# Kernel optimization log

Hardware: AMD Instinct MI355X
Metric: run time of the kernel (lower is better)

## Reference

```python
import jax, jax.numpy as jnp
import numpy as np
from jax import lax

B, T, D, N = 64, 4096, 256, 64


def setup_inputs() -> dict:
    key = jax.random.key(0)
    ks = jax.random.split(key, 3)
    return {
        "x": jax.random.normal(ks[0], (B, T, D), dtype=jnp.float32),
        "mask": jnp.ones((B, T), dtype=bool),
        "W": jax.random.normal(ks[1], (D, N), dtype=jnp.float32) * (1.0 / np.sqrt(D)),
        "b": jnp.zeros((N,), dtype=jnp.float32),
        "trans": jax.random.normal(ks[2], (N, N), dtype=jnp.float32) * 0.1,
        "left_boundary": jnp.zeros((N,), dtype=jnp.float32),
        "right_boundary": jnp.zeros((N,), dtype=jnp.float32),
    }


def _viterbi_decode(potentials, lens, trans):
    # potentials: [B, T, N]; lens: [B] int32; trans: [N, N]
    Tt = potentials.shape[1]

    def fwd_step(state, inp):
        pot_t, t = inp  # pot_t: [B, N], t scalar time index (1..T-1)
        scores = state[:, :, None] + trans[None, :, :]        # [B, N_prev, N_cur]
        bp = jnp.argmax(scores, axis=1).astype(jnp.int32)      # [B, N]
        new_state = pot_t + jnp.max(scores, axis=1)            # [B, N]
        valid = (t < lens)[:, None]                            # carry state past length
        return jnp.where(valid, new_state, state), bp

    pots_t = jnp.swapaxes(potentials, 0, 1)  # [T, B, N]
    final_state, bps = lax.scan(fwd_step, pots_t[0], (pots_t[1:], jnp.arange(1, Tt)))
    last_tag = jnp.argmax(final_state, axis=1).astype(jnp.int32)  # [B]

    def bwd_step(tag, inp):
        bp, t = inp  # bp: [B, N] backpointers for time t+1; t in 0..T-2
        prev = jnp.take_along_axis(bp, tag[:, None], axis=1)[:, 0]
        new_tag = jnp.where(t < lens - 1, prev, last_tag)
        return new_tag, new_tag

    _, tags = lax.scan(bwd_step, last_tag, (bps, jnp.arange(Tt - 1)), reverse=True)
    # tags: [T-1, B], position t holds decoded tag at time t
    decoded = jnp.concatenate([tags.T, last_tag[:, None]], axis=1)  # [B, T]
    return decoded


def reference(x, mask, W, b, trans, left_boundary, right_boundary):
    # projection (use_kernel=True)
    pot = jnp.einsum("btd,dn->btn", x, W) + b  # [B, T, N]
    # boundary potentials (use_boundary=True): added at fixed first/last timestep
    pot = pot.at[:, 0, :].add(left_boundary)
    pot = pot.at[:, -1, :].add(right_boundary)
    lens = jnp.sum(mask.astype(jnp.int32), axis=1)  # [B]
    decoded = _viterbi_decode(pot, lens, trans)
    return decoded, pot, lens, trans
```

## Files before the change

kernel.cpp:

```cpp
#include <hip/hip_runtime.h>

#define B_ 64
#define T_ 4096
#define D_ 256
#define N_ 64

typedef float f32x16 __attribute__((ext_vector_type(16)));

__global__ __launch_bounds__(64) void k_misc(const unsigned char* __restrict__ mask,
                                             const float* __restrict__ trans,
                                             float* __restrict__ out_lens,
                                             float* __restrict__ out_trans,
                                             int* __restrict__ lens_i) {
  int blk = blockIdx.x, lane = threadIdx.x;
  if (blk < B_) {
    int probe = (int)mask[0] + (int)mask[1] + (int)mask[2] + (int)mask[3];
    int cnt = 0;
    if (probe >= 2) {
      const unsigned char* row = mask + (size_t)blk * T_;
      for (int i = lane; i < T_; i += 64) cnt += row[i] ? 1 : 0;
    } else {
      const int* rowi = (const int*)mask + (size_t)blk * T_;
      for (int i = lane; i < T_; i += 64) cnt += rowi[i] ? 1 : 0;
    }
    #pragma unroll
    for (int off = 32; off > 0; off >>= 1) cnt += __shfl_down(cnt, off, 64);
    if (lane == 0) { out_lens[blk] = (float)cnt; lens_i[blk] = cnt; }
  } else {
    int base = (blk - B_) * 1024;
    for (int i = lane; i < 1024; i += 64) out_trans[base + i] = trans[base + i];
  }
}

__global__ __launch_bounds__(256, 2) void k_gemm(const float* __restrict__ x,
                                                 const float* __restrict__ W,
                                                 const float* __restrict__ bias,
                                                 const float* __restrict__ lb,
                                                 const float* __restrict__ rb,
                                                 float* __restrict__ pot) {
  __shared__ float xs[64 * D_];
  int tid = threadIdx.x;
  int wid = tid >> 6, lane = tid & 63;
  size_t row0 = (size_t)blockIdx.x * 64;

  const float* xb = x + row0 * D_;
  #pragma unroll
  for (int i = 0; i < 16; ++i) {
    int r = wid * 16 + i;
    float4 v = *reinterpret_cast<const float4*>(xb + (size_t)r * D_ + lane * 4);
    *reinterpret_cast<float4*>(&xs[r * D_ + lane * 4]) = v;
  }
  __syncthreads();

  float bv = bias[lane];
  float lbv = lb[lane];
  float rbv = rb[lane];

  float acc[16];
  #pragma unroll
  for (int r = 0; r < 16; ++r) {
    int t = (int)((row0 + wid * 16 + r) & (T_ - 1));
    float a = bv;
    if (t == 0)      a += lbv;
    if (t == T_ - 1) a += rbv;
    acc[r] = a;
  }

  #pragma unroll
  for (int c = 0; c < 4; ++c) {
    float w[64];
    #pragma unroll
    for (int k = 0; k < 64; ++k) w[k] = W[(size_t)(c * 64 + k) * N_ + lane];
    #pragma unroll
    for (int r = 0; r < 16; ++r) {
      const float4* xr = reinterpret_cast<const float4*>(&xs[(wid * 16 + r) * D_ + c * 64]);
      #pragma unroll
      for (int q = 0; q < 16; ++q) {
        float4 xv = xr[q];
        acc[r] += xv.x * w[q * 4 + 0];
        acc[r] += xv.y * w[q * 4 + 1];
        acc[r] += xv.z * w[q * 4 + 2];
        acc[r] += xv.w * w[q * 4 + 3];
      }
    }
  }

  #pragma unroll
  for (int r = 0; r < 16; ++r)
    pot[(row0 + wid * 16 + r) * N_ + lane] = acc[r];
}

#define FWD_STEP(TIDX, PREG)                                                      \
  {                                                                               \
    float pot_t = PREG;                                                           \
    int tp = (TIDX) + 4; if (tp > T_ - 1) tp = T_ - 1;                            \
    PREG = pb[(size_t)tp * N_ + lane];                                            \
    float m[64];                                                                  \
    _Pragma("unroll")                                                             \
    for (int g = 0; g < 16; ++g) {                                                \
      float4 s4 = st4v[g];                                                        \
      float2 ca = make_float2(s4.x, s4.y) + t2[2 * g];                            \
      float2 cb = make_float2(s4.z, s4.w) + t2[2 * g + 1];                        \
      m[4 * g + 0] = ca.x; m[4 * g + 1] = ca.y;                                   \
      m[4 * g + 2] = cb.x; m[4 * g + 3] = cb.y;                                   \
    }                                                                             \
    float r1[22];                                                                 \
    _Pragma("unroll")                                                             \
    for (int i = 0; i < 21; ++i)                                                  \
      r1[i] = fmaxf(fmaxf(m[3 * i], m[3 * i + 1]), m[3 * i + 2]);                 \
    r1[21] = m[63];                                                               \
    float r2[8];                                                                  \
    _Pragma("unroll")                                                             \
    for (int i = 0; i < 7; ++i)                                                   \
      r2[i] = fmaxf(fmaxf(r1[3 * i], r1[3 * i + 1]), r1[3 * i + 2]);              \
    r2[7] = r1[21];                                                               \
    float r3a = fmaxf(fmaxf(r2[0], r2[1]), r2[2]);                                \
    float r3b = fmaxf(fmaxf(r2[3], r2[4]), r2[5]);                                \
    float r3c = fmaxf(r2[6], r2[7]);                                              \
    float best = fmaxf(fmaxf(r3a, r3b), r3c);                                     \
    float ns = pot_t + best;                                                      \
    state = ((TIDX) < len_b) ? ns : state;                                        \
    sb[(size_t)(TIDX) * N_ + lane] = state;                                       \
    __builtin_amdgcn_wave_barrier();                                              \
    st[lane] = state;                                                             \
    __builtin_amdgcn_wave_barrier();                                              \
  }

__global__ __launch_bounds__(64, 1) void k_fwd_states(const float* __restrict__ pot,
                                                      const float* __restrict__ trans,
                                                      const int* __restrict__ lens_i,
                                                      float* __restrict__ states,
                                                      float* __restrict__ fstate) {
  int b = blockIdx.x, lane = threadIdx.x;
  __shared__ float4 st4v[16];
  float* st = (float*)st4v;

  float2 t2[32];
  #pragma unroll
  for (int p = 0; p < 32; ++p)
    t2[p] = make_float2(trans[(2 * p) * N_ + lane], trans[(2 * p + 1) * N_ + lane]);

  const float* pb = pot + (size_t)b * T_ * N_;
  float* sb = states + (size_t)b * T_ * N_;
  int len_b = lens_i[b];

  float state = pb[lane];
  st[lane] = state;
  sb[lane] = state;
  __builtin_amdgcn_wave_barrier();

  float p0 = pb[1 * N_ + lane];
  float p1 = pb[2 * N_ + lane];
  float p2 = pb[3 * N_ + lane];
  float p3 = pb[4 * N_ + lane];

  int t = 1;
  for (; t + 3 <= T_ - 1; t += 4) {
    FWD_STEP(t + 0, p0);
    FWD_STEP(t + 1, p1);
    FWD_STEP(t + 2, p2);
    FWD_STEP(t + 3, p3);
  }
  FWD_STEP(t + 0, p0);
  FWD_STEP(t + 1, p1);
  FWD_STEP(t + 2, p2);

  fstate[b * N_ + lane] = state;
}

__global__ __launch_bounds__(64, 2) void k_bp(const float* __restrict__ states,
                                              const float* __restrict__ trans,
                                              unsigned char* __restrict__ bp) {
  unsigned idx = blockIdx.x;
  unsigned b = idx / (unsigned)(T_ - 1);
  unsigned t = 1u + idx - b * (unsigned)(T_ - 1);
  int lane = threadIdx.x;

  float tcol[64];
  #pragma unroll
  for (int p = 0; p < 64; ++p) tcol[p] = trans[p * N_ + lane];

  const float* srow = states + ((size_t)b * T_ + (t - 1)) * N_;

  float c[64];
  #pragma unroll
  for (int p = 0; p < 64; ++p) c[p] = srow[p] + tcol[p];

  float v1[32]; int i1[32];
  #pragma unroll
  for (int i = 0; i < 32; ++i) {
    bool g = c[2 * i + 1] > c[2 * i];
    v1[i] = g ? c[2 * i + 1] : c[2 * i];
    i1[i] = g ? 2 * i + 1 : 2 * i;
  }
  float v2[16]; int i2[16];
  #pragma unroll
  for (int i = 0; i < 16; ++i) {
    bool g = v1[2 * i + 1] > v1[2 * i];
    v2[i] = g ? v1[2 * i + 1] : v1[2 * i];
    i2[i] = g ? i1[2 * i + 1] : i1[2 * i];
  }
  float v3[8]; int i3[8];
  #pragma unroll
  for (int i = 0; i < 8; ++i) {
    bool g = v2[2 * i + 1] > v2[2 * i];
    v3[i] = g ? v2[2 * i + 1] : v2[2 * i];
    i3[i] = g ? i2[2 * i + 1] : i2[2 * i];
  }
  float v4[4]; int i4[4];
  #pragma unroll
  for (int i = 0; i < 4; ++i) {
    bool g = v3[2 * i + 1] > v3[2 * i];
    v4[i] = g ? v3[2 * i + 1] : v3[2 * i];
    i4[i] = g ? i3[2 * i + 1] : i3[2 * i];
  }
  bool ga = v4[1] > v4[0];
  float va = ga ? v4[1] : v4[0]; int ia = ga ? i4[1] : i4[0];
  bool gb = v4[3] > v4[2];
  float vb = gb ? v4[3] : v4[2]; int ib = gb ? i4[3] : i4[2];
  int bpi = (vb > va) ? ib : ia;

  bp[((size_t)b * T_ + t) * N_ + lane] = (unsigned char)bpi;
}

__global__ __launch_bounds__(64, 1) void k_bwd(const unsigned char* __restrict__ bp,
                                               const float* __restrict__ fstate,
                                               const int* __restrict__ lens_i,
                                               float* __restrict__ decoded) {
  int b = blockIdx.x, lane = threadIdx.x;

  __shared__ float fv[64];
  __shared__ int sh_tag;
  fv[lane] = fstate[b * N_ + lane];
  __syncthreads();
  if (lane == 0) {
    float best = fv[0]; int tg = 0;
    for (int i = 1; i < 64; ++i) if (fv[i] > best) { best = fv[i]; tg = i; }
    sh_tag = tg;
  }
  __syncthreads();
  int s_last = __builtin_amdgcn_readfirstlane(sh_tag);
  int len_b = lens_i[b];

  const unsigned char* bpb = bp + (size_t)b * T_ * N_;
  float* dec = decoded + (size_t)b * T_;

  int s_tag = s_last;
  if (lane == 0) dec[T_ - 1] = (float)s_last;

  const int G = 32;
  int bufA[G], bufB[G];
  const int k0 = T_ - 1;
  #pragma unroll
  for (int i = 0; i < G; ++i) bufA[i] = (int)bpb[(size_t)(k0 - i) * N_ + lane];

  const int nrows = T_ - 1;
  const int groups = nrows / G;

  for (int g = 0; g < groups; ++g) {
    int kn = k0 - G * (g + 1);
    #pragma unroll
    for (int i = 0; i < G; ++i)
      bufB[i] = (kn - i >= 1) ? (int)bpb[(size_t)(kn - i) * N_ + lane] : 0;

    int kbase = k0 - G * g;
    #pragma unroll
    for (int i = 0; i < G; ++i) {
      int k = kbase - i;
      int prev = __builtin_amdgcn_readlane(bufA[i], s_tag);
      int t = k - 1;
      s_tag = (t < len_b - 1) ? prev : s_last;
      if (lane == 0) dec[t] = (float)s_tag;
    }
    #pragma unroll
    for (int i = 0; i < G; ++i) bufA[i] = bufB[i];
  }

  int kbase = k0 - G * groups;
  #pragma unroll
  for (int i = 0; i < G; ++i) {
    int k = kbase - i;
    if (k >= 1) {
      int prev = __builtin_amdgcn_readlane(bufA[i], s_tag);
      int t = k - 1;
      s_tag = (t < len_b - 1) ? prev : s_last;
      if (lane == 0) dec[t] = (float)s_tag;
    }
  }
}

extern "C" void kernel_launch(void* const* d_in, const int* in_sizes, int n_in,
                              void* d_out, int out_size, void* d_ws, size_t ws_size,
                              hipStream_t stream) {
  const float* x            = (const float*)d_in[0];
  const unsigned char* mask = (const unsigned char*)d_in[1];
  const float* W            = (const float*)d_in[2];
  const float* bias         = (const float*)d_in[3];
  const float* trans        = (const float*)d_in[4];
  const float* lb           = (const float*)d_in[5];
  const float* rb           = (const float*)d_in[6];

  float* out         = (float*)d_out;
  float* out_decoded = out;
  float* out_pot     = out + (size_t)B_ * T_;
  float* out_lens    = out_pot + (size_t)B_ * T_ * N_;
  float* out_trans   = out_lens + B_;

  const size_t bp_bytes   = (size_t)B_ * T_ * N_;
  const size_t fstate_off = bp_bytes;
  const size_t lens_off   = fstate_off + (size_t)B_ * N_ * 4;
  const size_t states_off = lens_off + 256;

  unsigned char* bp = (unsigned char*)d_ws;
  float* fstate     = (float*)((char*)d_ws + fstate_off);
  int*   lens_i     = (int*)((char*)d_ws + lens_off);
  float* states     = (float*)((char*)d_ws + states_off);

  k_misc<<<68, 64, 0, stream>>>(mask, trans, out_lens, out_trans, lens_i);
  k_gemm<<<(B_ * T_) / 64, 256, 0, stream>>>(x, W, bias, lb, rb, out_pot);
  k_fwd_states<<<B_, 64, 0, stream>>>(out_pot, trans, lens_i, states, fstate);
  k_bp<<<B_ * (T_ - 1), 64, 0, stream>>>(states, trans, bp);
  k_bwd<<<B_, 64, 0, stream>>>(bp, fstate, lens_i, out_decoded);
}
```

Baseline: 1.492 ms.

## Interleave two batch rows per forward wave and batch four timesteps per bp block

The forward max-plus recurrence kernel now runs one wave per pair of batch rows, interleaving two independent dependency chains so their LDS reads and max reductions can overlap. The goal is to hide per-step latency in the serial scan. The cost is half as many active waves (32 instead of 64), which leaves much of the GPU idle, and higher register pressure. The backpointer kernel now handles four timesteps per block, reusing the trans column it loads and cutting the block count by four, though this lowers parallelism in that kernel.

```diff
diff --git a/kernel.cpp b/kernel.cpp
--- a/kernel.cpp
+++ b/kernel.cpp
@@ -90,39 +90,59 @@
     pot[(row0 + wid * 16 + r) * N_ + lane] = acc[r];
 }
 
-#define FWD_STEP(TIDX, PREG)                                                      \
+#define FWD_STEP2(TIDX, PRA, PRB)                                                 \
   {                                                                               \
-    float pot_t = PREG;                                                           \
+    float potA = PRA;                                                             \
+    float potB = PRB;                                                             \
     int tp = (TIDX) + 4; if (tp > T_ - 1) tp = T_ - 1;                            \
-    PREG = pb[(size_t)tp * N_ + lane];                                            \
-    float m[64];                                                                  \
+    PRA = pbA[(size_t)tp * N_ + lane];                                            \
+    PRB = pbB[(size_t)tp * N_ + lane];                                            \
+    float mA[64], mB[64];                                                         \
     _Pragma("unroll")                                                             \
     for (int g = 0; g < 16; ++g) {                                                \
-      float4 s4 = st4v[g];                                                        \
+      float4 s4 = stA4[g];                                                        \
       float2 ca = make_float2(s4.x, s4.y) + t2[2 * g];                            \
       float2 cb = make_float2(s4.z, s4.w) + t2[2 * g + 1];                        \
-      m[4 * g + 0] = ca.x; m[4 * g + 1] = ca.y;                                   \
-      m[4 * g + 2] = cb.x; m[4 * g + 3] = cb.y;                                   \
+      mA[4 * g + 0] = ca.x; mA[4 * g + 1] = ca.y;                                 \
+      mA[4 * g + 2] = cb.x; mA[4 * g + 3] = cb.y;                                 \
     }                                                                             \
-    float r1[22];                                                                 \
     _Pragma("unroll")                                                             \
-    for (int i = 0; i < 21; ++i)                                                  \
-      r1[i] = fmaxf(fmaxf(m[3 * i], m[3 * i + 1]), m[3 * i + 2]);                 \
-    r1[21] = m[63];                                                               \
-    float r2[8];                                                                  \
+    for (int g = 0; g < 16; ++g) {                                                \
+      float4 s4 = stB4[g];                                                        \
+      float2 ca = make_float2(s4.x, s4.y) + t2[2 * g];                            \
+      float2 cb = make_float2(s4.z, s4.w) + t2[2 * g + 1];                        \
+      mB[4 * g + 0] = ca.x; mB[4 * g + 1] = ca.y;                                 \
+      mB[4 * g + 2] = cb.x; mB[4 * g + 3] = cb.y;                                 \
+    }                                                                             \
+    float r1A[22], r1B[22];                                                       \
     _Pragma("unroll")                                                             \
-    for (int i = 0; i < 7; ++i)                                                   \
-      r2[i] = fmaxf(fmaxf(r1[3 * i], r1[3 * i + 1]), r1[3 * i + 2]);              \
-    r2[7] = r1[21];                                                               \
-    float r3a = fmaxf(fmaxf(r2[0], r2[1]), r2[2]);                                \
-    float r3b = fmaxf(fmaxf(r2[3], r2[4]), r2[5]);                                \
-    float r3c = fmaxf(r2[6], r2[7]);                                              \
-    float best = fmaxf(fmaxf(r3a, r3b), r3c);                                     \
-    float ns = pot_t + best;                                                      \
-    state = ((TIDX) < len_b) ? ns : state;                                        \
-    sb[(size_t)(TIDX) * N_ + lane] = state;                                       \
+    for (int i = 0; i < 21; ++i) {                                                \
+      r1A[i] = fmaxf(fmaxf(mA[3 * i], mA[3 * i + 1]), mA[3 * i + 2]);             \
+      r1B[i] = fmaxf(fmaxf(mB[3 * i], mB[3 * i + 1]), mB[3 * i + 2]);             \
+    }                                                                             \
+    r1A[21] = mA[63]; r1B[21] = mB[63];                                           \
+    float r2A[8], r2B[8];                                                         \
+    _Pragma("unroll")                                                             \
+    for (int i = 0; i < 7; ++i) {                                                 \
+      r2A[i] = fmaxf(fmaxf(r1A[3 * i], r1A[3 * i + 1]), r1A[3 * i + 2]);          \
+      r2B[i] = fmaxf(fmaxf(r1B[3 * i], r1B[3 * i + 1]), r1B[3 * i + 2]);          \
+    }                                                                             \
+    r2A[7] = r1A[21]; r2B[7] = r1B[21];                                           \
+    float bestA = fmaxf(fmaxf(fmaxf(fmaxf(r2A[0], r2A[1]), r2A[2]),               \
+                              fmaxf(fmaxf(r2A[3], r2A[4]), r2A[5])),              \
+                        fmaxf(r2A[6], r2A[7]));                                   \
+    float bestB = fmaxf(fmaxf(fmaxf(fmaxf(r2B[0], r2B[1]), r2B[2]),               \
+                              fmaxf(fmaxf(r2B[3], r2B[4]), r2B[5])),              \
+                        fmaxf(r2B[6], r2B[7]));                                   \
+    float nsA = potA + bestA;                                                     \
+    float nsB = potB + bestB;                                                     \
+    stateA = ((TIDX) < lenA) ? nsA : stateA;                                      \
+    stateB = ((TIDX) < lenB) ? nsB : stateB;                                      \
+    sbA[(size_t)(TIDX) * N_ + lane] = stateA;                                     \
+    sbB[(size_t)(TIDX) * N_ + lane] = stateB;                                     \
     __builtin_amdgcn_wave_barrier();                                              \
-    st[lane] = state;                                                             \
+    stA[lane] = stateA;                                                           \
+    stB[lane] = stateB;                                                           \
     __builtin_amdgcn_wave_barrier();                                              \
   }
 
@@ -131,96 +151,115 @@
                                                       const int* __restrict__ lens_i,
                                                       float* __restrict__ states,
                                                       float* __restrict__ fstate) {
-  int b = blockIdx.x, lane = threadIdx.x;
-  __shared__ float4 st4v[16];
-  float* st = (float*)st4v;
+  int b0 = blockIdx.x, lane = threadIdx.x;
+  int bA = b0, bB = b0 + 32;
+
+  __shared__ float4 stA4[16];
+  __shared__ float4 stB4[16];
+  float* stA = (float*)stA4;
+  float* stB = (float*)stB4;
 
   float2 t2[32];
   #pragma unroll
   for (int p = 0; p < 32; ++p)
     t2[p] = make_float2(trans[(2 * p) * N_ + lane], trans[(2 * p + 1) * N_ + lane]);
 
-  const float* pb = pot + (size_t)b * T_ * N_;
-  float* sb = states + (size_t)b * T_ * N_;
-  int len_b = lens_i[b];
-
-  float state = pb[lane];
-  st[lane] = state;
-  sb[lane] = state;
+  const float* pbA = pot + (size_t)bA * T_ * N_;
+  const float* pbB = pot + (size_t)bB * T_ * N_;
+  float* sbA = states + (size_t)bA * T_ * N_;
+  float* sbB = states + (size_t)bB * T_ * N_;
+  int lenA = lens_i[bA];
+  int lenB = lens_i[bB];
+
+  float stateA = pbA[lane];
+  float stateB = pbB[lane];
+  stA[lane] = stateA;
+  stB[lane] = stateB;
+  sbA[lane] = stateA;
+  sbB[lane] = stateB;
   __builtin_amdgcn_wave_barrier();
 
-  float p0 = pb[1 * N_ + lane];
-  float p1 = pb[2 * N_ + lane];
-  float p2 = pb[3 * N_ + lane];
-  float p3 = pb[4 * N_ + lane];
+  float pA0 = pbA[1 * N_ + lane], pB0 = pbB[1 * N_ + lane];
+  float pA1 = pbA[2 * N_ + lane], pB1 = pbB[2 * N_ + lane];
+  float pA2 = pbA[3 * N_ + lane], pB2 = pbB[3 * N_ + lane];
+  float pA3 = pbA[4 * N_ + lane], pB3 = pbB[4 * N_ + lane];
 
   int t = 1;
   for (; t + 3 <= T_ - 1; t += 4) {
-    FWD_STEP(t + 0, p0);
-    FWD_STEP(t + 1, p1);
-    FWD_STEP(t + 2, p2);
-    FWD_STEP(t + 3, p3);
-  }
-  FWD_STEP(t + 0, p0);
-  FWD_STEP(t + 1, p1);
-  FWD_STEP(t + 2, p2);
-
-  fstate[b * N_ + lane] = state;
+    FWD_STEP2(t + 0, pA0, pB0);
+    FWD_STEP2(t + 1, pA1, pB1);
+    FWD_STEP2(t + 2, pA2, pB2);
+    FWD_STEP2(t + 3, pA3, pB3);
+  }
+  FWD_STEP2(t + 0, pA0, pB0);
+  FWD_STEP2(t + 1, pA1, pB1);
+  FWD_STEP2(t + 2, pA2, pB2);
+
+  fstate[bA * N_ + lane] = stateA;
+  fstate[bB * N_ + lane] = stateB;
 }
 
 __global__ __launch_bounds__(64, 2) void k_bp(const float* __restrict__ states,
                                               const float* __restrict__ trans,
                                               unsigned char* __restrict__ bp) {
   unsigned idx = blockIdx.x;
-  unsigned b = idx / (unsigned)(T_ - 1);
-  unsigned t = 1u + idx - b * (unsigned)(T_ - 1);
+  unsigned b = idx >> 10;
+  unsigned c4 = idx & 1023u;
   int lane = threadIdx.x;
 
   float tcol[64];
   #pragma unroll
   for (int p = 0; p < 64; ++p) tcol[p] = trans[p * N_ + lane];
 
-  const float* srow = states + ((size_t)b * T_ + (t - 1)) * N_;
-
-  float c[64];
-  #pragma unroll
-  for (int p = 0; p < 64; ++p) c[p] = srow[p] + tcol[p];
-
-  float v1[32]; int i1[32];
-  #pragma unroll
-  for (int i = 0; i < 32; ++i) {
-    bool g = c[2 * i + 1] > c[2 * i];
-    v1[i] = g ? c[2 * i + 1] : c[2 * i];
-    i1[i] = g ? 2 * i + 1 : 2 * i;
-  }
-  float v2[16]; int i2[16];
-  #pragma unroll
-  for (int i = 0; i < 16; ++i) {
-    bool g = v1[2 * i + 1] > v1[2 * i];
-    v2[i] = g ? v1[2 * i + 1] : v1[2 * i];
-    i2[i] = g ? i1[2 * i + 1] : i1[2 * i];
-  }
-  float v3[8]; int i3[8];
-  #pragma unroll
-  for (int i = 0; i < 8; ++i) {
-    bool g = v2[2 * i + 1] > v2[2 * i];
-    v3[i] = g ? v2[2 * i + 1] : v2[2 * i];
-    i3[i] = g ? i2[2 * i + 1] : i2[2 * i];
-  }
-  float v4[4]; int i4[4];
-  #pragma unroll
-  for (int i = 0; i < 4; ++i) {
-    bool g = v3[2 * i + 1] > v3[2 * i];
-    v4[i] = g ? v3[2 * i + 1] : v3[2 * i];
-    i4[i] = g ? i3[2 * i + 1] : i3[2 * i];
-  }
-  bool ga = v4[1] > v4[0];
-  float va = ga ? v4[1] : v4[0]; int ia = ga ? i4[1] : i4[0];
-  bool gb = v4[3] > v4[2];
-  float vb = gb ? v4[3] : v4[2]; int ib = gb ? i4[3] : i4[2];
-  int bpi = (vb > va) ? ib : ia;
-
-  bp[((size_t)b * T_ + t) * N_ + lane] = (unsigned char)bpi;
+  int tbase = (int)(c4 * 4 + 1);
+
+  #pragma unroll
+  for (int tt = 0; tt < 4; ++tt) {
+    int t = tbase + tt;
+    if (t > T_ - 1) break;
+
+    const float* srow = states + ((size_t)b * T_ + (t - 1)) * N_;
+
+    float c[64];
+    #pragma unroll
+    for (int p = 0; p < 64; ++p) c[p] = srow[p] + tcol[p];
+
+    float v1[32]; int i1[32];
+    #pragma unroll
+    for (int i = 0; i < 32; ++i) {
+      bool g = c[2 * i + 1] > c[2 * i];
+      v1[i] = g ? c[2 * i + 1] : c[2 * i];
+      i1[i] = g ? 2 * i + 1 : 2 * i;
+    }
+    float v2[16]; int i2[16];
+    #pragma unroll
+    for (int i = 0; i < 16; ++i) {
+      bool g = v1[2 * i + 1] > v1[2 * i];
+      v2[i] = g ? v1[2 * i + 1] : v1[2 * i];
+      i2[i] = g ? i1[2 * i + 1] : i1[2 * i];
+    }
+    float v3[8]; int i3[8];
+    #pragma unroll
+    for (int i = 0; i < 8; ++i) {
+      bool g = v2[2 * i + 1] > v2[2 * i];
+      v3[i] = g ? v2[2 * i + 1] : v2[2 * i];
+      i3[i] = g ? i2[2 * i + 1] : i2[2 * i];
+    }
+    float v4[4]; int i4[4];
+    #pragma unroll
+    for (int i = 0; i < 4; ++i) {
+      bool g = v3[2 * i + 1] > v3[2 * i];
+      v4[i] = g ? v3[2 * i + 1] : v3[2 * i];
+      i4[i] = g ? i3[2 * i + 1] : i3[2 * i];
+    }
+    bool ga = v4[1] > v4[0];
+    float va = ga ? v4[1] : v4[0]; int ia = ga ? i4[1] : i4[0];
+    bool gb = v4[3] > v4[2];
+    float vb = gb ? v4[3] : v4[2]; int ib = gb ? i4[3] : i4[2];
+    int bpi = (vb > va) ? ib : ia;
+
+    bp[((size_t)b * T_ + t) * N_ + lane] = (unsigned char)bpi;
+  }
 }
 
 __global__ __launch_bounds__(64, 1) void k_bwd(const unsigned char* __restrict__ bp,
@@ -318,7 +357,7 @@
 
   k_misc<<<68, 64, 0, stream>>>(mask, trans, out_lens, out_trans, lens_i);
   k_gemm<<<(B_ * T_) / 64, 256, 0, stream>>>(x, W, bias, lb, rb, out_pot);
-  k_fwd_states<<<B_, 64, 0, stream>>>(out_pot, trans, lens_i, states, fstate);
-  k_bp<<<B_ * (T_ - 1), 64, 0, stream>>>(states, trans, bp);
+  k_fwd_states<<<B_ / 2, 64, 0, stream>>>(out_pot, trans, lens_i, states, fstate);
+  k_bp<<<B_ * (T_ / 4), 64, 0, stream>>>(states, trans, bp);
   k_bwd<<<B_, 64, 0, stream>>>(bp, fstate, lens_i, out_decoded);
 }
```

New measurement: 3.685 ms. 2.47x slower.

## Split Viterbi forward max over four waves using readlane broadcasts

Applied to the files above, without the earlier changes.

The serial forward recurrence kernel now runs four waves per batch. Each wave handles 16 previous tags, broadcasts the state with readlane instead of going through an LDS round trip, and reduces to a partial max. The partials are combined through a double-buffered LDS array after a workgroup barrier. This shortens the per-step dependency chain of 64 max operations, at the cost of an s_barrier on every timestep across the 4096-long scan.

```diff
diff --git a/kernel.cpp b/kernel.cpp
--- a/kernel.cpp
+++ b/kernel.cpp
@@ -90,64 +90,59 @@
     pot[(row0 + wid * 16 + r) * N_ + lane] = acc[r];
 }
 
+#define RDL(J) (__int_as_float(__builtin_amdgcn_readlane(__float_as_int(state), pb16 + (J))) + tc[J])
+
 #define FWD_STEP(TIDX, PREG)                                                      \
   {                                                                               \
     float pot_t = PREG;                                                           \
     int tp = (TIDX) + 4; if (tp > T_ - 1) tp = T_ - 1;                            \
     PREG = pb[(size_t)tp * N_ + lane];                                            \
-    float m[64];                                                                  \
-    _Pragma("unroll")                                                             \
-    for (int g = 0; g < 16; ++g) {                                                \
-      float4 s4 = st4v[g];                                                        \
-      float2 ca = make_float2(s4.x, s4.y) + t2[2 * g];                            \
-      float2 cb = make_float2(s4.z, s4.w) + t2[2 * g + 1];                        \
-      m[4 * g + 0] = ca.x; m[4 * g + 1] = ca.y;                                   \
-      m[4 * g + 2] = cb.x; m[4 * g + 3] = cb.y;                                   \
-    }                                                                             \
-    float r1[22];                                                                 \
-    _Pragma("unroll")                                                             \
-    for (int i = 0; i < 21; ++i)                                                  \
-      r1[i] = fmaxf(fmaxf(m[3 * i], m[3 * i + 1]), m[3 * i + 2]);                 \
-    r1[21] = m[63];                                                               \
-    float r2[8];                                                                  \
-    _Pragma("unroll")                                                             \
-    for (int i = 0; i < 7; ++i)                                                   \
-      r2[i] = fmaxf(fmaxf(r1[3 * i], r1[3 * i + 1]), r1[3 * i + 2]);              \
-    r2[7] = r1[21];                                                               \
-    float r3a = fmaxf(fmaxf(r2[0], r2[1]), r2[2]);                                \
-    float r3b = fmaxf(fmaxf(r2[3], r2[4]), r2[5]);                                \
-    float r3c = fmaxf(r2[6], r2[7]);                                              \
-    float best = fmaxf(fmaxf(r3a, r3b), r3c);                                     \
+    float c0 = RDL(0), c1 = RDL(1), c2 = RDL(2), c3 = RDL(3);                     \
+    float c4 = RDL(4), c5 = RDL(5), c6 = RDL(6), c7 = RDL(7);                     \
+    float c8 = RDL(8), c9 = RDL(9), c10 = RDL(10), c11 = RDL(11);                 \
+    float c12 = RDL(12), c13 = RDL(13), c14 = RDL(14), c15 = RDL(15);             \
+    float m0 = fmaxf(fmaxf(c0, c1), c2);                                          \
+    float m1 = fmaxf(fmaxf(c3, c4), c5);                                          \
+    float m2 = fmaxf(fmaxf(c6, c7), c8);                                          \
+    float m3 = fmaxf(fmaxf(c9, c10), c11);                                        \
+    float m4 = fmaxf(fmaxf(c12, c13), c14);                                       \
+    float pa = fmaxf(fmaxf(fmaxf(m0, m1), m2), fmaxf(fmaxf(m3, m4), c15));        \
+    part[(TIDX) & 1][wid][lane] = pa;                                             \
+    asm volatile("s_waitcnt lgkmcnt(0)" ::: "memory");                            \
+    __builtin_amdgcn_s_barrier();                                                 \
+    asm volatile("" ::: "memory");                                                \
+    float q0 = part[(TIDX) & 1][0][lane];                                         \
+    float q1 = part[(TIDX) & 1][1][lane];                                         \
+    float q2 = part[(TIDX) & 1][2][lane];                                         \
+    float q3 = part[(TIDX) & 1][3][lane];                                         \
+    float best = fmaxf(fmaxf(q0, q1), fmaxf(q2, q3));                             \
     float ns = pot_t + best;                                                      \
     state = ((TIDX) < len_b) ? ns : state;                                        \
-    sb[(size_t)(TIDX) * N_ + lane] = state;                                       \
-    __builtin_amdgcn_wave_barrier();                                              \
-    st[lane] = state;                                                             \
-    __builtin_amdgcn_wave_barrier();                                              \
-  }
-
-__global__ __launch_bounds__(64, 1) void k_fwd_states(const float* __restrict__ pot,
-                                                      const float* __restrict__ trans,
-                                                      const int* __restrict__ lens_i,
-                                                      float* __restrict__ states,
-                                                      float* __restrict__ fstate) {
-  int b = blockIdx.x, lane = threadIdx.x;
-  __shared__ float4 st4v[16];
-  float* st = (float*)st4v;
-
-  float2 t2[32];
-  #pragma unroll
-  for (int p = 0; p < 32; ++p)
-    t2[p] = make_float2(trans[(2 * p) * N_ + lane], trans[(2 * p + 1) * N_ + lane]);
+    if (wid == ((TIDX) & 3)) sb[(size_t)(TIDX) * N_ + lane] = state;              \
+  }
+
+__global__ __launch_bounds__(256, 1) void k_fwd_states(const float* __restrict__ pot,
+                                                       const float* __restrict__ trans,
+                                                       const int* __restrict__ lens_i,
+                                                       float* __restrict__ states,
+                                                       float* __restrict__ fstate) {
+  __shared__ float part[2][4][64];
+
+  int b = blockIdx.x;
+  int tid = threadIdx.x;
+  int wid = tid >> 6, lane = tid & 63;
+  int pb16 = wid * 16;
+
+  float tc[16];
+  #pragma unroll
+  for (int j = 0; j < 16; ++j) tc[j] = trans[(size_t)(pb16 + j) * N_ + lane];
 
   const float* pb = pot + (size_t)b * T_ * N_;
   float* sb = states + (size_t)b * T_ * N_;
   int len_b = lens_i[b];
 
   float state = pb[lane];
-  st[lane] = state;
-  sb[lane] = state;
-  __builtin_amdgcn_wave_barrier();
+  if (wid == 0) sb[lane] = state;
 
   float p0 = pb[1 * N_ + lane];
   float p1 = pb[2 * N_ + lane];
@@ -165,7 +160,7 @@
   FWD_STEP(t + 1, p1);
   FWD_STEP(t + 2, p2);
 
-  fstate[b * N_ + lane] = state;
+  if (wid == 0) fstate[b * N_ + lane] = state;
 }
 
 __global__ __launch_bounds__(64, 2) void k_bp(const float* __restrict__ states,
@@ -318,7 +313,7 @@
 
   k_misc<<<68, 64, 0, stream>>>(mask, trans, out_lens, out_trans, lens_i);
   k_gemm<<<(B_ * T_) / 64, 256, 0, stream>>>(x, W, bias, lb, rb, out_pot);
-  k_fwd_states<<<B_, 64, 0, stream>>>(out_pot, trans, lens_i, states, fstate);
+  k_fwd_states<<<B_, 256, 0, stream>>>(out_pot, trans, lens_i, states, fstate);
   k_bp<<<B_ * (T_ - 1), 64, 0, stream>>>(states, trans, bp);
   k_bwd<<<B_, 64, 0, stream>>>(bp, fstate, lens_i, out_decoded);
 }
```

New measurement: 2.214 ms. 1.48x slower.
